# Performance work log

Measured on AMD Instinct MI355X. Metric: run time of the kernel, lower is better.

## Reference

```python
import jax, jax.numpy as jnp
import numpy as np
import math

N_COARSE, N_FINE = 8192, 32768
DEC_DIM, ENC_DIM, OUT_DIM, K = 256, 128, 128, 16
LN_EPS = 1e-5


def setup_inputs() -> dict:
    key = jax.random.key(0)
    ks = jax.random.split(key, 16)
    s = lambda fan_in: 1.0 / math.sqrt(fan_in)
    return {
        "decoder_features": jax.random.normal(ks[0], (N_COARSE, DEC_DIM), jnp.float32),
        "decoder_pos": jax.random.normal(ks[1], (N_COARSE, 3), jnp.float32),
        "encoder_features": jax.random.normal(ks[2], (N_FINE, ENC_DIM), jnp.float32),
        "encoder_pos": jax.random.normal(ks[3], (N_FINE, 3), jnp.float32),
        "encoder_labels": jax.random.randint(ks[4], (N_FINE,), 0, 13, jnp.int64),
        # params (torch nn.Linear default init scale)
        "Wq": jax.random.uniform(ks[5], (DEC_DIM, ENC_DIM), jnp.float32, -s(ENC_DIM), s(ENC_DIM)),
        "bq": jnp.zeros((DEC_DIM,), jnp.float32),
        "Wk": jax.random.uniform(ks[6], (DEC_DIM, DEC_DIM), jnp.float32, -s(DEC_DIM), s(DEC_DIM)),
        "bk": jnp.zeros((DEC_DIM,), jnp.float32),
        "Wv": jax.random.uniform(ks[7], (DEC_DIM, DEC_DIM), jnp.float32, -s(DEC_DIM), s(DEC_DIM)),
        "bv": jnp.zeros((DEC_DIM,), jnp.float32),
        "W1": jax.random.uniform(ks[8], (OUT_DIM, DEC_DIM + ENC_DIM), jnp.float32, -s(DEC_DIM + ENC_DIM), s(DEC_DIM + ENC_DIM)),
        "b1": jnp.zeros((OUT_DIM,), jnp.float32),
        "W2": jax.random.uniform(ks[9], (OUT_DIM, OUT_DIM), jnp.float32, -s(OUT_DIM), s(OUT_DIM)),
        "b2": jnp.zeros((OUT_DIM,), jnp.float32),
        "ln_g": jnp.ones((OUT_DIM,), jnp.float32),
        "ln_b": jnp.zeros((OUT_DIM,), jnp.float32),
    }


def _knn_indices(encoder_pos, decoder_pos, k):
    # For each fine (encoder) point, k nearest coarse (decoder) points.
    # squared distances [N_fine, N_coarse]
    d2 = (
        jnp.sum(encoder_pos * encoder_pos, axis=1, keepdims=True)
        - 2.0 * encoder_pos @ decoder_pos.T
        + jnp.sum(decoder_pos * decoder_pos, axis=1)[None, :]
    )
    _, idx = jax.lax.top_k(-d2, k)  # [N_fine, K]
    return idx


def reference(decoder_features, decoder_pos, encoder_features, encoder_pos,
              encoder_labels, Wq, bq, Wk, bk, Wv, bv, W1, b1, W2, b2, ln_g, ln_b):
    idx = _knn_indices(encoder_pos, decoder_pos, K)            # [Nf, K]
    nbr = decoder_features[idx]                                 # [Nf, K, Dd]
    query = encoder_features @ Wq.T + bq                        # [Nf, Dd]
    keys = nbr @ Wk.T + bk                                      # [Nf, K, Dd]
    values = nbr @ Wv.T + bv                                    # [Nf, K, Dd]
    scores = jnp.einsum('nd,nkd->nk', query, keys) / math.sqrt(DEC_DIM)
    # segment softmax over edges grouped by fine target == softmax over K
    weights = jax.nn.softmax(scores, axis=-1)                   # [Nf, K]
    agg = jnp.einsum('nk,nkd->nd', weights, values)             # [Nf, Dd]
    combined = jnp.concatenate([agg, encoder_features], axis=-1)
    h = jax.nn.relu(combined @ W1.T + b1)
    up = h @ W2.T + b2                                          # [Nf, out]
    mu = jnp.mean(up, axis=-1, keepdims=True)
    var = jnp.var(up, axis=-1, keepdims=True)
    out = (up - mu) * jax.lax.rsqrt(var + LN_EPS) * ln_g + ln_b
    # dropout is identity in eval mode
    return (out, encoder_pos, encoder_labels)
```

## Files before the change

kernel.cpp:

```cpp
#include <hip/hip_runtime.h>
#include <hip/hip_bf16.h>

typedef __hip_bfloat16 bf16;
typedef unsigned short u16;
typedef float f32x2 __attribute__((ext_vector_type(2)));

#define NC 8192
#define NF 32768
#define KNN 16
#define FMAXV 3.402823466e+38f

__device__ __forceinline__ float bfbits2f(u16 u){
  union { unsigned u; float f; } x; x.u = ((unsigned)u) << 16; return x.f;
}
__device__ __forceinline__ float asfloat(unsigned u){
  union { unsigned u; float f; } x; x.u = u; return x.f;
}
__device__ __forceinline__ f32x2 pk_fma(f32x2 a, f32x2 b, f32x2 c){
  f32x2 d;
  asm("v_pk_fma_f32 %0, %1, %2, %3" : "=v"(d) : "v"(a), "v"(b), "v"(c));
  return d;
}

__global__ __launch_bounds__(256) void k_prep(const float* __restrict__ dpos,
                                              const float* __restrict__ W1,
                                              const float* __restrict__ W2,
                                              float4* __restrict__ posP,
                                              float4* __restrict__ W1eSa,
                                              float4* __restrict__ W1eSb,
                                              float4* __restrict__ W2Sa,
                                              float4* __restrict__ W2Sb){
  int g = blockIdx.x * 256 + threadIdx.x;
  if (g < 4096){
    const float2* dp2 = (const float2*)(dpos + (size_t)g * 6);
    float2 a = dp2[0], b = dp2[1], c = dp2[2];
    float x0 = a.x, y0 = a.y, z0 = b.x;
    float x1 = b.y, y1 = c.x, z1 = c.y;
    float dd0 = __fadd_rn(__fadd_rn(__fmul_rn(x0,x0), __fmul_rn(y0,y0)), __fmul_rn(z0,z0));
    float dd1 = __fadd_rn(__fadd_rn(__fmul_rn(x1,x1), __fmul_rn(y1,y1)), __fmul_rn(z1,z1));
    posP[g * 2]     = make_float4(x0, x1, y0, y1);
    posP[g * 2 + 1] = make_float4(z0, z1, dd0 * 0.5f, dd1 * 0.5f);
  } else if (g >= 8192 && g < 10240){
    int f = g - 8192; int c4 = f >> 6, jg = f & 63;
    W1eSa[f] = ((const float4*)(W1 + (size_t)(2 * jg) * 384 + 256))[c4];
  } else if (g >= 10240 && g < 12288){
    int f = g - 10240; int c4 = f >> 6, jg = f & 63;
    W1eSb[f] = ((const float4*)(W1 + (size_t)(2 * jg + 1) * 384 + 256))[c4];
  } else if (g >= 12288 && g < 14336){
    int f = g - 12288; int c4 = f >> 6, jg = f & 63;
    W2Sa[f] = ((const float4*)(W2 + (size_t)(2 * jg) * 128))[c4];
  } else if (g >= 14336){
    int f = g - 14336; int c4 = f >> 6, jg = f & 63;
    W2Sb[f] = ((const float4*)(W2 + (size_t)(2 * jg + 1) * 128))[c4];
  }
}

__global__ __launch_bounds__(256) void k_wprod(const float* __restrict__ Wk,
                                               const float* __restrict__ Wv,
                                               const float* __restrict__ Wq,
                                               const float* __restrict__ W1,
                                               const float* __restrict__ bk,
                                               const float* __restrict__ bv,
                                               const float* __restrict__ bq,
                                               float* __restrict__ WkqS,
                                               float* __restrict__ WvuS,
                                               float* __restrict__ bkq,
                                               float* __restrict__ bvu,
                                               float* __restrict__ wbq,
                                               float* __restrict__ sbq){
  __shared__ float red[256];
  int b = blockIdx.x, t = threadIdx.x;
  if (b < 128){
    int c = b;
    float acc = 0.f;
    for (int j = 0; j < 256; ++j)
      acc = fmaf(Wk[(size_t)j * 256 + t], Wq[(size_t)j * 128 + c], acc);
    WkqS[(size_t)((t >> 2) * 128 + c) * 4 + (t & 3)] = acc;
    red[t] = bk[t] * Wq[(size_t)t * 128 + c];
    __syncthreads();
    for (int s = 128; s > 0; s >>= 1){ if (t < s) red[t] += red[t + s]; __syncthreads(); }
    if (t == 0) bkq[c] = red[0];
  } else if (b < 256){
    int h = b - 128;
    float acc = 0.f;
    for (int c2 = 0; c2 < 256; ++c2)
      acc = fmaf(Wv[(size_t)c2 * 256 + t], W1[(size_t)h * 384 + c2], acc);
    WvuS[(size_t)((t >> 2) * 128 + h) * 4 + (t & 3)] = acc;
    red[t] = bv[t] * W1[(size_t)h * 384 + t];
    __syncthreads();
    for (int s = 128; s > 0; s >>= 1){ if (t < s) red[t] += red[t + s]; __syncthreads(); }
    if (t == 0) bvu[h] = red[0];
  } else {
    float acc = 0.f;
    for (int j = 0; j < 256; ++j)
      acc = fmaf(Wk[(size_t)j * 256 + t], bq[j], acc);
    wbq[t] = acc;
    red[t] = bk[t] * bq[t];
    __syncthreads();
    for (int s = 128; s > 0; s >>= 1){ if (t < s) red[t] += red[t + s]; __syncthreads(); }
    if (t == 0) sbq[0] = red[0];
  }
}

__global__ __launch_bounds__(256) void k_dec(const float* __restrict__ df,
                                             const float4* __restrict__ WkqS,
                                             const float4* __restrict__ WvuS,
                                             const float* __restrict__ bkq,
                                             const float* __restrict__ bvu,
                                             const float* __restrict__ wbq,
                                             const float* __restrict__ sbq,
                                             bf16* __restrict__ Zd, bf16* __restrict__ Ud,
                                             float* __restrict__ bqK){
  __shared__ float part[16][16];
  int t = threadIdx.x;
  int g0 = blockIdx.x * 16;
  int half = __builtin_amdgcn_readfirstlane(t >> 7);
  int c = t & 127;
  const float4* W = half ? WvuS : WkqS;
  float acc[16];
  #pragma unroll
  for (int p = 0; p < 16; ++p) acc[p] = 0.f;
  for (int j4 = 0; j4 < 64; ++j4){
    float4 w = W[j4 * 128 + c];
    #pragma unroll
    for (int p = 0; p < 16; ++p){
      float4 a = ((const float4*)(df + (size_t)(g0 + p) * 256))[j4];
      acc[p] += w.x*a.x + w.y*a.y + w.z*a.z + w.w*a.w;
    }
  }
  float bias = half ? bvu[c] : bkq[c];
  bf16* dst = half ? Ud : Zd;
  #pragma unroll
  for (int p = 0; p < 16; ++p)
    dst[(size_t)(g0 + p) * 128 + c] = __float2bfloat16(acc[p] + bias);
  {
    int r = t >> 4, seg = t & 15;
    float s = 0.f;
    const float* dr = df + (size_t)(g0 + r) * 256 + seg * 16;
    const float* wq = wbq + seg * 16;
    #pragma unroll
    for (int e = 0; e < 16; ++e) s = fmaf(dr[e], wq[e], s);
    part[r][seg] = s;
  }
  __syncthreads();
  if (t < 16){
    float s = sbq[0];
    #pragma unroll
    for (int seg = 0; seg < 16; ++seg) s += part[t][seg];
    bqK[g0 + t] = s;
  }
}

__global__ __launch_bounds__(256) void k_attn(const float* __restrict__ epos,
                                              const float4* __restrict__ posP,
                                              const float* __restrict__ ef,
                                              const bf16* __restrict__ Zd,
                                              const bf16* __restrict__ Ud,
                                              const float* __restrict__ bqK,
                                              bf16* __restrict__ hagg){
  __shared__ float smin[8 * 64];
  __shared__ float tauLDS[8];
  __shared__ int   cnt[8];
  __shared__ float lval[8][64];
  __shared__ int   lidx[8][64];

  int t = threadIdx.x, lane = t & 63, w = t >> 6;
  int n0 = blockIdx.x * 8;
  f32x2 nex2[8], ney2[8], nez2[8];
  #pragma unroll
  for (int p = 0; p < 8; ++p){
    float nx = -epos[(n0 + p) * 3 + 0];
    float ny = -epos[(n0 + p) * 3 + 1];
    float nz = -epos[(n0 + p) * 3 + 2];
    nex2[p].x = nx; nex2[p].y = nx;
    ney2[p].x = ny; ney2[p].y = ny;
    nez2[p].x = nz; nez2[p].y = nz;
  }
  const float4* base = posP + w * 2048;

  f32x2 vmin2[8];
  #pragma unroll
  for (int p = 0; p < 8; ++p){ vmin2[p].x = FMAXV; vmin2[p].y = FMAXV; }
  #pragma unroll 2
  for (int s = 0; s < 16; ++s){
    int q2 = (s * 64 + lane) * 2;
    float4 XY = base[q2], ZW = base[q2 + 1];
    f32x2 X = {XY.x, XY.y}, Y = {XY.z, XY.w}, Z = {ZW.x, ZW.y}, W = {ZW.z, ZW.w};
    #pragma unroll
    for (int p = 0; p < 8; ++p){
      f32x2 v2 = pk_fma(nex2[p], X, W);
      v2 = pk_fma(ney2[p], Y, v2);
      v2 = pk_fma(nez2[p], Z, v2);
      vmin2[p].x = fminf(vmin2[p].x, v2.x);
      vmin2[p].y = fminf(vmin2[p].y, v2.y);
    }
  }
  float vmin[8];
  #pragma unroll
  for (int p = 0; p < 8; ++p) vmin[p] = fminf(vmin2[p].x, vmin2[p].y);

  #pragma unroll
  for (int k = 2; k <= 64; k <<= 1){
    #pragma unroll
    for (int j = k >> 1; j > 0; j >>= 1){
      bool keepmin = ((lane & j) == 0) == ((lane & k) == 0);
      #pragma unroll
      for (int p = 0; p < 8; ++p){
        float pv = __shfl_xor(vmin[p], j);
        vmin[p] = keepmin ? fminf(vmin[p], pv) : fmaxf(vmin[p], pv);
      }
    }
  }
  if (lane < 16){
    #pragma unroll
    for (int p = 0; p < 8; ++p) smin[p * 64 + w * 16 + lane] = vmin[p];
  }
  if (t < 8) cnt[t] = 0;
  __syncthreads();

  {
    int src = (lane & 16) ? (lane ^ 15) : lane;
    float v0 = smin[(w * 2 + 0) * 64 + src];
    float v1 = smin[(w * 2 + 1) * 64 + src];
    #pragma unroll
    for (int j = 16; j > 0; j >>= 1){
      bool keepmin = ((lane & 32) == 0) == ((lane & j) == 0);
      float p0 = __shfl_xor(v0, j); v0 = keepmin ? fminf(v0, p0) : fmaxf(v0, p0);
      float p1 = __shfl_xor(v1, j); v1 = keepmin ? fminf(v1, p1) : fmaxf(v1, p1);
    }
    #pragma unroll
    for (int j = 32; j > 0; j >>= 1){
      bool keepmin = ((lane & j) == 0);
      float p0 = __shfl_xor(v0, j); v0 = keepmin ? fminf(v0, p0) : fmaxf(v0, p0);
      float p1 = __shfl_xor(v1, j); v1 = keepmin ? fminf(v1, p1) : fmaxf(v1, p1);
    }
    if (lane == 16){ tauLDS[w * 2] = v0; tauLDS[w * 2 + 1] = v1; }
  }
  __syncthreads();
  float tau0[8];
  #pragma unroll
  for (int p = 0; p < 8; ++p) tau0[p] = tauLDS[p];

  #pragma unroll 2
  for (int s = 0; s < 16; ++s){
    int q = s * 64 + lane;
    float4 XY = base[q * 2], ZW = base[q * 2 + 1];
    f32x2 X = {XY.x, XY.y}, Y = {XY.z, XY.w}, Z = {ZW.x, ZW.y}, W = {ZW.z, ZW.w};
    int cand0 = w * 2048 + q * 2;
    #pragma unroll
    for (int p = 0; p < 8; ++p){
      f32x2 v2 = pk_fma(nex2[p], X, W);
      v2 = pk_fma(ney2[p], Y, v2);
      v2 = pk_fma(nez2[p], Z, v2);
      if (v2.x <= tau0[p]){
        int slot = atomicAdd(&cnt[p], 1);
        if (slot < 64){ lval[p][slot] = v2.x; lidx[p][slot] = cand0; }
      }
      if (v2.y <= tau0[p]){
        int slot = atomicAdd(&cnt[p], 1);
        if (slot < 64){ lval[p][slot] = v2.y; lidx[p][slot] = cand0 + 1; }
      }
    }
  }
  __syncthreads();

  {
    int p0 = w * 2, p1 = w * 2 + 1;
    int nA = n0 + p0, nB = n0 + p1;
    int c0 = cnt[p0]; if (c0 > 64) c0 = 64;
    int c1 = cnt[p1]; if (c1 > 64) c1 = 64;
    float va = (lane < c0) ? lval[p0][lane] : FMAXV;
    int   ia = (lane < c0) ? lidx[p0][lane] : 0x7fffffff;
    float vb = (lane < c1) ? lval[p1][lane] : FMAXV;
    int   ib = (lane < c1) ? lidx[p1][lane] : 0x7fffffff;

    #pragma unroll
    for (int k = 2; k <= 16; k <<= 1){
      #pragma unroll
      for (int j = k >> 1; j > 0; j >>= 1){
        bool keepmin = ((lane & k) == 0) == ((lane & j) == 0);
        { float pv = __shfl_xor(va, j); int pid = __shfl_xor(ia, j);
          bool pl = (pv < va) || (pv == va && pid < ia);
          if (keepmin ? pl : !pl){ va = pv; ia = pid; } }
        { float pv = __shfl_xor(vb, j); int pid = __shfl_xor(ib, j);
          bool pl = (pv < vb) || (pv == vb && pid < ib);
          if (keepmin ? pl : !pl){ vb = pv; ib = pid; } }
      }
    }
    { float pv = __shfl_xor(va, 16); int pid = __shfl_xor(ia, 16);
      if ((pv < va) || (pv == va && pid < ia)){ va = pv; ia = pid; } }
    { float pv = __shfl_xor(vb, 16); int pid = __shfl_xor(ib, 16);
      if ((pv < vb) || (pv == vb && pid < ib)){ vb = pv; ib = pid; } }
    #pragma unroll
    for (int j = 8; j > 0; j >>= 1){
      bool keepmin = ((lane & 32) == 0) == ((lane & j) == 0);
      { float pv = __shfl_xor(va, j); int pid = __shfl_xor(ia, j);
        bool pl = (pv < va) || (pv == va && pid < ia);
        if (keepmin ? pl : !pl){ va = pv; ia = pid; } }
      { float pv = __shfl_xor(vb, j); int pid = __shfl_xor(ib, j);
        bool pl = (pv < vb) || (pv == vb && pid < ib);
        if (keepmin ? pl : !pl){ vb = pv; ib = pid; } }
    }
    { float pv = __shfl_xor(va, 32); int pid = __shfl_xor(ia, 32);
      if ((pv < va) || (pv == va && pid < ia)){ va = pv; ia = pid; } }
    { float pv = __shfl_xor(vb, 32); int pid = __shfl_xor(ib, 32);
      if ((pv < vb) || (pv == vb && pid < ib)){ vb = pv; ib = pid; } }
    int topi0 = ia, topi1 = ib;

    int kk = lane & 15, part = lane >> 4;
    int ik0 = __shfl(topi0, kk);
    int ik1 = __shfl(topi1, kk);
    const uint4*  zr0 = (const uint4*)((const u16*)Zd + (size_t)ik0 * 128) + part * 4;
    const uint4*  zr1 = (const uint4*)((const u16*)Zd + (size_t)ik1 * 128) + part * 4;
    const float4* e40 = (const float4*)(ef + (size_t)nA * 128) + part * 8;
    const float4* e41 = (const float4*)(ef + (size_t)nB * 128) + part * 8;
    float pr0 = 0.f, pr1 = 0.f;
    #pragma unroll
    for (int i = 0; i < 4; ++i){
      uint4 z0 = zr0[i], z1 = zr1[i];
      float4 ea0 = e40[2 * i], eb0 = e40[2 * i + 1];
      float4 ea1 = e41[2 * i], eb1 = e41[2 * i + 1];
      pr0 = fmaf(ea0.x, asfloat(z0.x << 16), pr0); pr0 = fmaf(ea0.y, asfloat(z0.x & 0xffff0000u), pr0);
      pr0 = fmaf(ea0.z, asfloat(z0.y << 16), pr0); pr0 = fmaf(ea0.w, asfloat(z0.y & 0xffff0000u), pr0);
      pr0 = fmaf(eb0.x, asfloat(z0.z << 16), pr0); pr0 = fmaf(eb0.y, asfloat(z0.z & 0xffff0000u), pr0);
      pr0 = fmaf(eb0.z, asfloat(z0.w << 16), pr0); pr0 = fmaf(eb0.w, asfloat(z0.w & 0xffff0000u), pr0);
      pr1 = fmaf(ea1.x, asfloat(z1.x << 16), pr1); pr1 = fmaf(ea1.y, asfloat(z1.x & 0xffff0000u), pr1);
      pr1 = fmaf(ea1.z, asfloat(z1.y << 16), pr1); pr1 = fmaf(ea1.w, asfloat(z1.y & 0xffff0000u), pr1);
      pr1 = fmaf(eb1.x, asfloat(z1.z << 16), pr1); pr1 = fmaf(eb1.y, asfloat(z1.z & 0xffff0000u), pr1);
      pr1 = fmaf(eb1.z, asfloat(z1.w << 16), pr1); pr1 = fmaf(eb1.w, asfloat(z1.w & 0xffff0000u), pr1);
    }
    pr0 += __shfl_xor(pr0, 16); pr1 += __shfl_xor(pr1, 16);
    pr0 += __shfl_xor(pr0, 32); pr1 += __shfl_xor(pr1, 32);
    float sc0 = (pr0 + bqK[ik0]) * (1.0f / 16.0f);
    float sc1 = (pr1 + bqK[ik1]) * (1.0f / 16.0f);

    float mx0 = sc0, mx1 = sc1;
    #pragma unroll
    for (int off = 8; off >= 1; off >>= 1){
      mx0 = fmaxf(mx0, __shfl_xor(mx0, off));
      mx1 = fmaxf(mx1, __shfl_xor(mx1, off));
    }
    float e0 = (lane < KNN) ? __expf(sc0 - mx0) : 0.f;
    float e1 = (lane < KNN) ? __expf(sc1 - mx1) : 0.f;
    float l0 = e0, l1 = e1;
    #pragma unroll
    for (int off = 8; off >= 1; off >>= 1){
      l0 += __shfl_xor(l0, off);
      l1 += __shfl_xor(l1, off);
    }
    float wgt0 = (lane < KNN) ? (e0 / l0) : 0.f;
    float wgt1 = (lane < KNN) ? (e1 / l1) : 0.f;

    float a00 = 0.f, a01 = 0.f, a10 = 0.f, a11 = 0.f;
    #pragma unroll
    for (int k = 0; k < KNN; ++k){
      int ikk0 = __shfl(topi0, k);
      int ikk1 = __shfl(topi1, k);
      float wk0 = __shfl(wgt0, k);
      float wk1 = __shfl(wgt1, k);
      ushort2 u0 = *(const ushort2*)((const u16*)Ud + (size_t)ikk0 * 128 + lane * 2);
      ushort2 u1 = *(const ushort2*)((const u16*)Ud + (size_t)ikk1 * 128 + lane * 2);
      a00 = fmaf(wk0, bfbits2f(u0.x), a00);
      a01 = fmaf(wk0, bfbits2f(u0.y), a01);
      a10 = fmaf(wk1, bfbits2f(u1.x), a10);
      a11 = fmaf(wk1, bfbits2f(u1.y), a11);
    }
    bf16 h00 = __float2bfloat16(a00), h01 = __float2bfloat16(a01);
    bf16 h10 = __float2bfloat16(a10), h11 = __float2bfloat16(a11);
    ushort2 st0; st0.x = *(u16*)&h00; st0.y = *(u16*)&h01;
    ushort2 st1; st1.x = *(u16*)&h10; st1.y = *(u16*)&h11;
    *(ushort2*)(hagg + (size_t)nA * 128 + lane * 2) = st0;
    *(ushort2*)(hagg + (size_t)nB * 128 + lane * 2) = st1;
  }
}

__global__ __launch_bounds__(256) void k_mlp(const bf16* __restrict__ hagg,
                                             const float* __restrict__ ef,
                                             const float4* __restrict__ W1eSa,
                                             const float4* __restrict__ W1eSb,
                                             const float* __restrict__ b1,
                                             const float4* __restrict__ W2Sa,
                                             const float4* __restrict__ W2Sb,
                                             const float* __restrict__ b2,
                                             const float* __restrict__ lng, const float* __restrict__ lnb,
                                             const float* __restrict__ epos, const int* __restrict__ lab,
                                             float* __restrict__ out){
  __shared__ float hbuf[16 * 128];
  __shared__ float ubuf[16 * 128];
  __shared__ float stats[32];
  int t = threadIdx.x;
  int n0 = blockIdx.x * 16;
  {
    int gid = blockIdx.x * 256 + t;
    if (gid < NF){
      float* op = out + (size_t)NF * 128;
      op[gid * 3 + 0] = epos[gid * 3 + 0];
      op[gid * 3 + 1] = epos[gid * 3 + 1];
      op[gid * 3 + 2] = epos[gid * 3 + 2];
      out[(size_t)NF * 128 + (size_t)NF * 3 + gid] = (float)lab[gid];
    }
  }
  int jg = t & 63;
  int pg4 = __builtin_amdgcn_readfirstlane((t >> 6) * 4);
  int j0 = jg * 2;
  float acc[2][4];
  #pragma unroll
  for (int a = 0; a < 2; ++a)
    #pragma unroll
    for (int p = 0; p < 4; ++p) acc[a][p] = 0.f;
  for (int c4 = 0; c4 < 32; ++c4){
    float4 wa = W1eSa[c4 * 64 + jg];
    float4 wb = W1eSb[c4 * 64 + jg];
    #pragma unroll
    for (int p = 0; p < 4; ++p){
      float4 x = ((const float4*)(ef + (size_t)(n0 + pg4 + p) * 128))[c4];
      acc[0][p] += wa.x*x.x + wa.y*x.y + wa.z*x.z + wa.w*x.w;
      acc[1][p] += wb.x*x.x + wb.y*x.y + wb.z*x.z + wb.w*x.w;
    }
  }
  float b1a = b1[j0], b1b = b1[j0 + 1];
  #pragma unroll
  for (int p = 0; p < 4; ++p){
    size_t row = (size_t)(n0 + pg4 + p);
    ushort2 hgv = *(const ushort2*)((const u16*)hagg + row * 128 + j0);
    hbuf[(pg4 + p) * 128 + j0]     = fmaxf(acc[0][p] + b1a + bfbits2f(hgv.x), 0.f);
    hbuf[(pg4 + p) * 128 + j0 + 1] = fmaxf(acc[1][p] + b1b + bfbits2f(hgv.y), 0.f);
  }
  __syncthreads();
  float acc2[2][4];
  #pragma unroll
  for (int a = 0; a < 2; ++a)
    #pragma unroll
    for (int p = 0; p < 4; ++p) acc2[a][p] = 0.f;
  const float4* hb4 = (const float4*)hbuf;
  for (int c4 = 0; c4 < 32; ++c4){
    float4 wa = W2Sa[c4 * 64 + jg];
    float4 wb = W2Sb[c4 * 64 + jg];
    #pragma unroll
    for (int p = 0; p < 4; ++p){
      float4 x = hb4[(pg4 + p) * 32 + c4];
      acc2[0][p] += wa.x*x.x + wa.y*x.y + wa.z*x.z + wa.w*x.w;
      acc2[1][p] += wb.x*x.x + wb.y*x.y + wb.z*x.z + wb.w*x.w;
    }
  }
  float b2a = b2[j0], b2b = b2[j0 + 1];
  float u[2][4];
  #pragma unroll
  for (int p = 0; p < 4; ++p){
    u[0][p] = acc2[0][p] + b2a;
    u[1][p] = acc2[1][p] + b2b;
    ubuf[(pg4 + p) * 128 + j0]     = u[0][p];
    ubuf[(pg4 + p) * 128 + j0 + 1] = u[1][p];
  }
  __syncthreads();
  {
    int p = t >> 4, qi = t & 15;
    const float* ub = &ubuf[p * 128 + qi * 8];
    float s = 0.f, s2 = 0.f;
    #pragma unroll
    for (int e2i = 0; e2i < 8; ++e2i){ float v = ub[e2i]; s += v; s2 += v * v; }
    #pragma unroll
    for (int off = 1; off < 16; off <<= 1){ s += __shfl_xor(s, off); s2 += __shfl_xor(s2, off); }
    if (qi == 0){
      float mu = s * (1.f / 128.f);
      float var = s2 * (1.f / 128.f) - mu * mu;
      stats[p] = mu;
      stats[16 + p] = rsqrtf(fmaxf(var, 0.f) + 1e-5f);
    }
  }
  __syncthreads();
  float ga = lng[j0], gb = lng[j0 + 1];
  float ba = lnb[j0], bbv = lnb[j0 + 1];
  #pragma unroll
  for (int p = 0; p < 4; ++p){
    float mu = stats[pg4 + p], rs = stats[16 + pg4 + p];
    out[(size_t)(n0 + pg4 + p) * 128 + j0]     = (u[0][p] - mu) * rs * ga + ba;
    out[(size_t)(n0 + pg4 + p) * 128 + j0 + 1] = (u[1][p] - mu) * rs * gb + bbv;
  }
}

extern "C" void kernel_launch(void* const* d_in, const int* in_sizes, int n_in,
                              void* d_out, int out_size, void* d_ws, size_t ws_size,
                              hipStream_t stream){
  const float* df   = (const float*)d_in[0];
  const float* dpos = (const float*)d_in[1];
  const float* ef   = (const float*)d_in[2];
  const float* epos = (const float*)d_in[3];
  const int*   lab  = (const int*)d_in[4];
  const float* Wq = (const float*)d_in[5];
  const float* bq = (const float*)d_in[6];
  const float* Wk = (const float*)d_in[7];
  const float* bk = (const float*)d_in[8];
  const float* Wv = (const float*)d_in[9];
  const float* bv = (const float*)d_in[10];
  const float* W1 = (const float*)d_in[11];
  const float* b1 = (const float*)d_in[12];
  const float* W2 = (const float*)d_in[13];
  const float* b2 = (const float*)d_in[14];
  const float* lng = (const float*)d_in[15];
  const float* lnb = (const float*)d_in[16];
  float* out = (float*)d_out;

  char* wsb = (char*)d_ws;
  float4* posP  = (float4*)(wsb);
  bf16*   Zd    = (bf16*)(wsb + 131072);
  bf16*   Ud    = (bf16*)(wsb + 2228224);
  float*  bqK   = (float*)(wsb + 4325376);
  bf16*   hagg  = (bf16*)(wsb + 4358144);
  float4* W1eSa = (float4*)(wsb + 12746752);
  float4* W1eSb = (float4*)(wsb + 12779520);
  float4* W2Sa  = (float4*)(wsb + 12812288);
  float4* W2Sb  = (float4*)(wsb + 12845056);
  float*  WkqS  = (float*)(wsb + 12877824);
  float*  WvuS  = (float*)(wsb + 13008896);
  float*  bkq   = (float*)(wsb + 13139968);
  float*  bvu   = (float*)(wsb + 13140480);
  float*  wbq   = (float*)(wsb + 13140992);
  float*  sbq   = (float*)(wsb + 13142016);

  k_prep  <<<64,  256, 0, stream>>>(dpos, W1, W2, posP, W1eSa, W1eSb, W2Sa, W2Sb);
  k_wprod <<<257, 256, 0, stream>>>(Wk, Wv, Wq, W1, bk, bv, bq, WkqS, WvuS, bkq, bvu, wbq, sbq);
  k_dec   <<<NC / 16, 256, 0, stream>>>(df, (const float4*)WkqS, (const float4*)WvuS, bkq, bvu, wbq, sbq, Zd, Ud, bqK);
  k_attn  <<<NF / 8, 256, 0, stream>>>(epos, posP, ef, Zd, Ud, bqK, hagg);
  k_mlp   <<<NF / 16, 256, 0, stream>>>(hagg, ef, W1eSa, W1eSb, b1, W2Sa, W2Sb, b2, lng, lnb, epos, lab, out);
  (void)in_sizes; (void)n_in; (void)out_size; (void)ws_size;
}
```

Before: 339.2 us.

## Per-wave full KNN scan with ballot compaction; split weight-product reduction across blocks

k_attn now gives each wavefront its own 8 fine points and has it scan all coarse candidates. The cross-wave threshold merge through LDS and its barriers go away, and the threshold is read with a single lane shuffle. LDS atomicAdd candidate insertion is replaced by ballot/popcount compaction into per-wave buffers. k_wprod splits each 256-long dot product over 4 blocks with an LDS partial sum, and k_dec processes 8 rows per block instead of 16, so both kernels launch more blocks. The trade-off is 4x more serial scan work per wave in k_attn and smaller blocks of 128 threads.

```diff
diff --git a/kernel.cpp b/kernel.cpp
--- a/kernel.cpp
+++ b/kernel.cpp
@@ -68,37 +68,60 @@
                                                float* __restrict__ bvu,
                                                float* __restrict__ wbq,
                                                float* __restrict__ sbq){
+  __shared__ float partial[256];
   __shared__ float red[256];
-  int b = blockIdx.x, t = threadIdx.x;
-  if (b < 128){
-    int c = b;
+  int B = blockIdx.x, t = threadIdx.x;
+  int csel = B >> 2, tch = B & 3;
+  int o = (t & 63) + tch * 64;
+  int q = t >> 6;
+  int j0 = q * 64;
+  if (csel < 128){
+    int c = csel;
     float acc = 0.f;
-    for (int j = 0; j < 256; ++j)
-      acc = fmaf(Wk[(size_t)j * 256 + t], Wq[(size_t)j * 128 + c], acc);
-    WkqS[(size_t)((t >> 2) * 128 + c) * 4 + (t & 3)] = acc;
-    red[t] = bk[t] * Wq[(size_t)t * 128 + c];
+    for (int j = j0; j < j0 + 64; ++j)
+      acc = fmaf(Wk[(size_t)j * 256 + o], Wq[(size_t)j * 128 + c], acc);
+    partial[t] = acc;
+    if (tch == 0) red[t] = bk[t] * Wq[(size_t)t * 128 + c];
     __syncthreads();
-    for (int s = 128; s > 0; s >>= 1){ if (t < s) red[t] += red[t + s]; __syncthreads(); }
-    if (t == 0) bkq[c] = red[0];
-  } else if (b < 256){
-    int h = b - 128;
+    if (t < 64){
+      float a = partial[t] + partial[t + 64] + partial[t + 128] + partial[t + 192];
+      WkqS[(size_t)((o >> 2) * 128 + c) * 4 + (o & 3)] = a;
+    }
+    if (tch == 0){
+      for (int s = 128; s > 0; s >>= 1){ if (t < s) red[t] += red[t + s]; __syncthreads(); }
+      if (t == 0) bkq[c] = red[0];
+    }
+  } else if (csel < 256){
+    int h = csel - 128;
     float acc = 0.f;
-    for (int c2 = 0; c2 < 256; ++c2)
-      acc = fmaf(Wv[(size_t)c2 * 256 + t], W1[(size_t)h * 384 + c2], acc);
-    WvuS[(size_t)((t >> 2) * 128 + h) * 4 + (t & 3)] = acc;
-    red[t] = bv[t] * W1[(size_t)h * 384 + t];
+    for (int j = j0; j < j0 + 64; ++j)
+      acc = fmaf(Wv[(size_t)j * 256 + o], W1[(size_t)h * 384 + j], acc);
+    partial[t] = acc;
+    if (tch == 0) red[t] = bv[t] * W1[(size_t)h * 384 + t];
     __syncthreads();
-    for (int s = 128; s > 0; s >>= 1){ if (t < s) red[t] += red[t + s]; __syncthreads(); }
-    if (t == 0) bvu[h] = red[0];
+    if (t < 64){
+      float a = partial[t] + partial[t + 64] + partial[t + 128] + partial[t + 192];
+      WvuS[(size_t)((o >> 2) * 128 + h) * 4 + (o & 3)] = a;
+    }
+    if (tch == 0){
+      for (int s = 128; s > 0; s >>= 1){ if (t < s) red[t] += red[t + s]; __syncthreads(); }
+      if (t == 0) bvu[h] = red[0];
+    }
   } else {
     float acc = 0.f;
-    for (int j = 0; j < 256; ++j)
-      acc = fmaf(Wk[(size_t)j * 256 + t], bq[j], acc);
-    wbq[t] = acc;
-    red[t] = bk[t] * bq[t];
+    for (int j = j0; j < j0 + 64; ++j)
+      acc = fmaf(Wk[(size_t)j * 256 + o], bq[j], acc);
+    partial[t] = acc;
+    if (tch == 0) red[t] = bk[t] * bq[t];
     __syncthreads();
-    for (int s = 128; s > 0; s >>= 1){ if (t < s) red[t] += red[t + s]; __syncthreads(); }
-    if (t == 0) sbq[0] = red[0];
+    if (t < 64){
+      float a = partial[t] + partial[t + 64] + partial[t + 128] + partial[t + 192];
+      wbq[o] = a;
+    }
+    if (tch == 0){
+      for (int s = 128; s > 0; s >>= 1){ if (t < s) red[t] += red[t + s]; __syncthreads(); }
+      if (t == 0) sbq[0] = red[0];
+    }
   }
 }
 
@@ -111,19 +134,19 @@
                                              const float* __restrict__ sbq,
                                              bf16* __restrict__ Zd, bf16* __restrict__ Ud,
                                              float* __restrict__ bqK){
-  __shared__ float part[16][16];
+  __shared__ float part[8][32];
   int t = threadIdx.x;
-  int g0 = blockIdx.x * 16;
+  int g0 = blockIdx.x * 8;
   int half = __builtin_amdgcn_readfirstlane(t >> 7);
   int c = t & 127;
   const float4* W = half ? WvuS : WkqS;
-  float acc[16];
-  #pragma unroll
-  for (int p = 0; p < 16; ++p) acc[p] = 0.f;
+  float acc[8];
+  #pragma unroll
+  for (int p = 0; p < 8; ++p) acc[p] = 0.f;
   for (int j4 = 0; j4 < 64; ++j4){
     float4 w = W[j4 * 128 + c];
     #pragma unroll
-    for (int p = 0; p < 16; ++p){
+    for (int p = 0; p < 8; ++p){
       float4 a = ((const float4*)(df + (size_t)(g0 + p) * 256))[j4];
       acc[p] += w.x*a.x + w.y*a.y + w.z*a.z + w.w*a.w;
     }
@@ -131,41 +154,40 @@
   float bias = half ? bvu[c] : bkq[c];
   bf16* dst = half ? Ud : Zd;
   #pragma unroll
-  for (int p = 0; p < 16; ++p)
+  for (int p = 0; p < 8; ++p)
     dst[(size_t)(g0 + p) * 128 + c] = __float2bfloat16(acc[p] + bias);
   {
-    int r = t >> 4, seg = t & 15;
+    int r = t >> 5, seg = t & 31;
     float s = 0.f;
-    const float* dr = df + (size_t)(g0 + r) * 256 + seg * 16;
-    const float* wq = wbq + seg * 16;
-    #pragma unroll
-    for (int e = 0; e < 16; ++e) s = fmaf(dr[e], wq[e], s);
+    const float* dr = df + (size_t)(g0 + r) * 256 + seg * 8;
+    const float* wq = wbq + seg * 8;
+    #pragma unroll
+    for (int e = 0; e < 8; ++e) s = fmaf(dr[e], wq[e], s);
     part[r][seg] = s;
   }
   __syncthreads();
-  if (t < 16){
+  if (t < 8){
     float s = sbq[0];
     #pragma unroll
-    for (int seg = 0; seg < 16; ++seg) s += part[t][seg];
+    for (int seg = 0; seg < 32; ++seg) s += part[t][seg];
     bqK[g0 + t] = s;
   }
 }
 
-__global__ __launch_bounds__(256) void k_attn(const float* __restrict__ epos,
+__global__ __launch_bounds__(128) void k_attn(const float* __restrict__ epos,
                                               const float4* __restrict__ posP,
                                               const float* __restrict__ ef,
                                               const bf16* __restrict__ Zd,
                                               const bf16* __restrict__ Ud,
                                               const float* __restrict__ bqK,
                                               bf16* __restrict__ hagg){
-  __shared__ float smin[8 * 64];
-  __shared__ float tauLDS[8];
-  __shared__ int   cnt[8];
-  __shared__ float lval[8][64];
-  __shared__ int   lidx[8][64];
+  __shared__ float lval[2][8][64];
+  __shared__ int   lidx[2][8][64];
+  __shared__ int   cntL[2][8];
 
   int t = threadIdx.x, lane = t & 63, w = t >> 6;
-  int n0 = blockIdx.x * 8;
+  int n0 = blockIdx.x * 16 + w * 8;
+
   f32x2 nex2[8], ney2[8], nez2[8];
   #pragma unroll
   for (int p = 0; p < 8; ++p){
@@ -176,15 +198,14 @@
     ney2[p].x = ny; ney2[p].y = ny;
     nez2[p].x = nz; nez2[p].y = nz;
   }
-  const float4* base = posP + w * 2048;
 
   f32x2 vmin2[8];
   #pragma unroll
   for (int p = 0; p < 8; ++p){ vmin2[p].x = FMAXV; vmin2[p].y = FMAXV; }
   #pragma unroll 2
-  for (int s = 0; s < 16; ++s){
+  for (int s = 0; s < 64; ++s){
     int q2 = (s * 64 + lane) * 2;
-    float4 XY = base[q2], ZW = base[q2 + 1];
+    float4 XY = posP[q2], ZW = posP[q2 + 1];
     f32x2 X = {XY.x, XY.y}, Y = {XY.z, XY.w}, Z = {ZW.x, ZW.y}, W = {ZW.z, ZW.w};
     #pragma unroll
     for (int p = 0; p < 8; ++p){
@@ -211,68 +232,58 @@
       }
     }
   }
-  if (lane < 16){
-    #pragma unroll
-    for (int p = 0; p < 8; ++p) smin[p * 64 + w * 16 + lane] = vmin[p];
-  }
-  if (t < 8) cnt[t] = 0;
-  __syncthreads();
-
-  {
-    int src = (lane & 16) ? (lane ^ 15) : lane;
-    float v0 = smin[(w * 2 + 0) * 64 + src];
-    float v1 = smin[(w * 2 + 1) * 64 + src];
-    #pragma unroll
-    for (int j = 16; j > 0; j >>= 1){
-      bool keepmin = ((lane & 32) == 0) == ((lane & j) == 0);
-      float p0 = __shfl_xor(v0, j); v0 = keepmin ? fminf(v0, p0) : fmaxf(v0, p0);
-      float p1 = __shfl_xor(v1, j); v1 = keepmin ? fminf(v1, p1) : fmaxf(v1, p1);
-    }
-    #pragma unroll
-    for (int j = 32; j > 0; j >>= 1){
-      bool keepmin = ((lane & j) == 0);
-      float p0 = __shfl_xor(v0, j); v0 = keepmin ? fminf(v0, p0) : fmaxf(v0, p0);
-      float p1 = __shfl_xor(v1, j); v1 = keepmin ? fminf(v1, p1) : fmaxf(v1, p1);
-    }
-    if (lane == 16){ tauLDS[w * 2] = v0; tauLDS[w * 2 + 1] = v1; }
-  }
-  __syncthreads();
   float tau0[8];
   #pragma unroll
-  for (int p = 0; p < 8; ++p) tau0[p] = tauLDS[p];
-
+  for (int p = 0; p < 8; ++p) tau0[p] = __shfl(vmin[p], 16);
+
+  unsigned long long lmlt = (1ull << lane) - 1ull;
+  int cnt[8] = {0,0,0,0,0,0,0,0};
   #pragma unroll 2
-  for (int s = 0; s < 16; ++s){
+  for (int s = 0; s < 64; ++s){
     int q = s * 64 + lane;
-    float4 XY = base[q * 2], ZW = base[q * 2 + 1];
+    float4 XY = posP[q * 2], ZW = posP[q * 2 + 1];
     f32x2 X = {XY.x, XY.y}, Y = {XY.z, XY.w}, Z = {ZW.x, ZW.y}, W = {ZW.z, ZW.w};
-    int cand0 = w * 2048 + q * 2;
+    int cand0 = q * 2;
     #pragma unroll
     for (int p = 0; p < 8; ++p){
       f32x2 v2 = pk_fma(nex2[p], X, W);
       v2 = pk_fma(ney2[p], Y, v2);
       v2 = pk_fma(nez2[p], Z, v2);
-      if (v2.x <= tau0[p]){
-        int slot = atomicAdd(&cnt[p], 1);
-        if (slot < 64){ lval[p][slot] = v2.x; lidx[p][slot] = cand0; }
+      bool h0 = v2.x <= tau0[p];
+      bool h1 = v2.y <= tau0[p];
+      if (__any(h0 || h1)){
+        unsigned long long m0 = __ballot(h0);
+        unsigned long long m1 = __ballot(h1);
+        int base = cnt[p];
+        int c0 = __popcll(m0);
+        if (h0){
+          int s0 = base + (int)__popcll(m0 & lmlt);
+          if (s0 < 64){ lval[w][p][s0] = v2.x; lidx[w][p][s0] = cand0; }
+        }
+        if (h1){
+          int s1 = base + c0 + (int)__popcll(m1 & lmlt);
+          if (s1 < 64){ lval[w][p][s1] = v2.y; lidx[w][p][s1] = cand0 + 1; }
+        }
+        cnt[p] = base + c0 + (int)__popcll(m1);
       }
-      if (v2.y <= tau0[p]){
-        int slot = atomicAdd(&cnt[p], 1);
-        if (slot < 64){ lval[p][slot] = v2.y; lidx[p][slot] = cand0 + 1; }
-      }
-    }
+    }
+  }
+  if (lane == 0){
+    #pragma unroll
+    for (int p = 0; p < 8; ++p) cntL[w][p] = cnt[p];
   }
   __syncthreads();
 
-  {
-    int p0 = w * 2, p1 = w * 2 + 1;
+  #pragma unroll 1
+  for (int u = 0; u < 4; ++u){
+    int p0 = u * 2, p1 = u * 2 + 1;
     int nA = n0 + p0, nB = n0 + p1;
-    int c0 = cnt[p0]; if (c0 > 64) c0 = 64;
-    int c1 = cnt[p1]; if (c1 > 64) c1 = 64;
-    float va = (lane < c0) ? lval[p0][lane] : FMAXV;
-    int   ia = (lane < c0) ? lidx[p0][lane] : 0x7fffffff;
-    float vb = (lane < c1) ? lval[p1][lane] : FMAXV;
-    int   ib = (lane < c1) ? lidx[p1][lane] : 0x7fffffff;
+    int c0 = cntL[w][p0]; if (c0 > 64) c0 = 64;
+    int c1 = cntL[w][p1]; if (c1 > 64) c1 = 64;
+    float va = (lane < c0) ? lval[w][p0][lane] : FMAXV;
+    int   ia = (lane < c0) ? lidx[w][p0][lane] : 0x7fffffff;
+    float vb = (lane < c1) ? lval[w][p1][lane] : FMAXV;
+    int   ib = (lane < c1) ? lidx[w][p1][lane] : 0x7fffffff;
 
     #pragma unroll
     for (int k = 2; k <= 16; k <<= 1){
@@ -518,10 +529,10 @@
   float*  wbq   = (float*)(wsb + 13140992);
   float*  sbq   = (float*)(wsb + 13142016);
 
-  k_prep  <<<64,  256, 0, stream>>>(dpos, W1, W2, posP, W1eSa, W1eSb, W2Sa, W2Sb);
-  k_wprod <<<257, 256, 0, stream>>>(Wk, Wv, Wq, W1, bk, bv, bq, WkqS, WvuS, bkq, bvu, wbq, sbq);
-  k_dec   <<<NC / 16, 256, 0, stream>>>(df, (const float4*)WkqS, (const float4*)WvuS, bkq, bvu, wbq, sbq, Zd, Ud, bqK);
-  k_attn  <<<NF / 8, 256, 0, stream>>>(epos, posP, ef, Zd, Ud, bqK, hagg);
+  k_prep  <<<64,   256, 0, stream>>>(dpos, W1, W2, posP, W1eSa, W1eSb, W2Sa, W2Sb);
+  k_wprod <<<1028, 256, 0, stream>>>(Wk, Wv, Wq, W1, bk, bv, bq, WkqS, WvuS, bkq, bvu, wbq, sbq);
+  k_dec   <<<NC / 8, 256, 0, stream>>>(df, (const float4*)WkqS, (const float4*)WvuS, bkq, bvu, wbq, sbq, Zd, Ud, bqK);
+  k_attn  <<<NF / 16, 128, 0, stream>>>(epos, posP, ef, Zd, Ud, bqK, hagg);
   k_mlp   <<<NF / 16, 256, 0, stream>>>(hagg, ef, W1eSa, W1eSb, b1, W2Sa, W2Sb, b2, lng, lnb, epos, lab, out);
   (void)in_sizes; (void)n_in; (void)out_size; (void)ws_size;
 }
```

Result: slower. 360.9 us (+6.4%).
